# Optimization experiments

Measured on AMD Instinct MI355X. Metric: run time of the kernel, lower is better.

The kernel has to match this reference:

```python
import jax, jax.numpy as jnp
import numpy as np

D_IN, D_OUT, RANK, N = 4096, 4096, 16, 8192


def _quantize_weight(w, bits):
    # round-to-nearest fake quantization, stored back as floats (as in the torch code)
    absmax = jnp.abs(w).max()
    scale = (2 ** (bits - 1) - 1) / absmax
    q = jnp.clip(jnp.round(w * scale), -2 ** (bits - 1), 2 ** (bits - 1) - 1)
    return q / scale


def _double_quantization(w, bits):
    absmax = jnp.abs(w).max()
    c1 = (2 ** (bits - 1) - 1) / absmax          # scalar fp32 scale
    q = jnp.clip(jnp.round(w * c1), -2 ** (bits - 1), 2 ** (bits - 1) - 1)
    return c1, q / c1                             # c_kbit_2 has same shape as w


def setup_inputs() -> dict:
    key = jax.random.key(0)
    kX, kW, kL1, kL2 = jax.random.split(key, 4)
    X = jax.random.normal(kX, (N, D_IN), dtype=jnp.float32)
    W0 = jax.random.normal(kW, (D_IN, D_OUT), dtype=jnp.float32)
    W_nf4 = _quantize_weight(W0, bits=4)
    c_fp32_1, c_kbit_2 = _double_quantization(W_nf4, bits=8)
    L1 = jax.random.normal(kL1, (D_IN, RANK), dtype=jnp.float32)
    L2 = jax.random.normal(kL2, (RANK, D_OUT), dtype=jnp.float32)
    return {"X": X, "W_nf4": W_nf4, "c_fp32_1": c_fp32_1,
            "c_kbit_2": c_kbit_2, "L1": L1, "L2": L2}


def reference(X, W_nf4, c_fp32_1, c_kbit_2, L1, L2):
    # dequantize: elementwise scalar * elementwise-tensor scaling of stored weight
    W = W_nf4 * c_fp32_1 * c_kbit_2               # [D_IN, D_OUT]
    # main GEMM + low-rank LoRA path, added in the epilogue
    Y = X @ W + (X @ L1) @ L2                     # [N, D_OUT]
    return Y
```

## Files before the change

### kernel.cpp

```cpp
#include <hip/hip_runtime.h>


#define M_ROWS 8192
#define K_DIM  4096
#define N_OUT  4096
#define CVT_BLOCKS 16384
#define WP_BLOCKS  4096

typedef float  f32x16 __attribute__((ext_vector_type(16)));
typedef float  f32x4  __attribute__((ext_vector_type(4)));
typedef __bf16 bf16x8 __attribute__((ext_vector_type(8)));
typedef unsigned short ushort8v __attribute__((ext_vector_type(8)));

__device__ float          Tg[(size_t)M_ROWS * 16];
__device__ unsigned short L1t[16 * K_DIM];
__device__ unsigned short L2t[N_OUT * 16];

__device__ __forceinline__ unsigned short f2bf(float f) {
    __bf16 h = (__bf16)f;
    union { __bf16 h; unsigned short u; } v; v.h = h;
    return v.u;
}

__global__ __launch_bounds__(256) void cvt_kernel(
        const float* __restrict__ X, ushort8v* __restrict__ Xh) {
    size_t tid = (size_t)blockIdx.x * 256 + threadIdx.x;
    const float4* xp = (const float4*)X;
    float4 a = xp[tid * 2];
    float4 b = xp[tid * 2 + 1];
    ushort8v o;
    o[0] = f2bf(a.x); o[1] = f2bf(a.y); o[2] = f2bf(a.z); o[3] = f2bf(a.w);
    o[4] = f2bf(b.x); o[5] = f2bf(b.y); o[6] = f2bf(b.z); o[7] = f2bf(b.w);
    Xh[tid] = o;
}

__global__ __launch_bounds__(256) void wprep_kernel(
        const float* __restrict__ Wnf4, const float* __restrict__ c1p,
        const float* __restrict__ c2,   unsigned short* __restrict__ Wt) {
    __shared__ unsigned short tile[64][72];
    const int t  = threadIdx.x;
    const int wb = blockIdx.x;
    const int n0 = (wb & 63) * 64;
    const int k0 = (wb >> 6) * 64;
    const float c1 = *c1p;

    #pragma unroll
    for (int i = 0; i < 4; ++i) {
        int idx = i * 1024 + t * 4;
        int k = idx >> 6, n4 = idx & 63;
        size_t g = (size_t)(k0 + k) * N_OUT + n0 + n4;
        float4 w = *(const float4*)&Wnf4[g];
        float4 s = *(const float4*)&c2[g];
        tile[n4    ][k] = f2bf(w.x * c1 * s.x);
        tile[n4 + 1][k] = f2bf(w.y * c1 * s.y);
        tile[n4 + 2][k] = f2bf(w.z * c1 * s.z);
        tile[n4 + 3][k] = f2bf(w.w * c1 * s.w);
    }
    __syncthreads();

    #pragma unroll
    for (int i = 0; i < 2; ++i) {
        int task = i * 256 + t;
        int n = task >> 3, k8 = (task & 7) * 8;
        ushort8v o = *(const ushort8v*)&tile[n][k8];
        *(ushort8v*)&Wt[(size_t)(n0 + n) * K_DIM + k0 + k8] = o;
    }
}

__global__ __launch_bounds__(256) void lorap_kernel(
        const float* __restrict__ L1, const float* __restrict__ L2) {
    const int idx = blockIdx.x * 256 + threadIdx.x;
    if (idx < K_DIM) {
        const float4* lp = (const float4*)&L1[(size_t)idx * 16];
        float4 r0 = lp[0], r1 = lp[1], r2 = lp[2], r3 = lp[3];
        float v[16] = {r0.x, r0.y, r0.z, r0.w, r1.x, r1.y, r1.z, r1.w,
                       r2.x, r2.y, r2.z, r2.w, r3.x, r3.y, r3.z, r3.w};
        #pragma unroll
        for (int r = 0; r < 16; ++r)
            L1t[(size_t)r * K_DIM + idx] = f2bf(v[r]);
    } else {
        const int n = idx - K_DIM;
        ushort8v a, b;
        #pragma unroll
        for (int r = 0; r < 8; ++r) a[r] = f2bf(L2[(size_t)r * N_OUT + n]);
        #pragma unroll
        for (int r = 0; r < 8; ++r) b[r] = f2bf(L2[(size_t)(r + 8) * N_OUT + n]);
        *(ushort8v*)&L2t[(size_t)n * 16]     = a;
        *(ushort8v*)&L2t[(size_t)n * 16 + 8] = b;
    }
}

__global__ __launch_bounds__(256) void xl1_kernel(const __bf16* __restrict__ Xh) {
    __shared__ float red[4][256];
    const int m0 = blockIdx.x * 16;
    const int t = threadIdx.x, wv = t >> 6, lane = t & 63;
    const int l15 = lane & 15, l4 = lane >> 4;
    const __bf16* ap = Xh + (size_t)(m0 + l15) * K_DIM + wv * 1024 + l4 * 8;
    const __bf16* bp = (const __bf16*)L1t + (size_t)l15 * K_DIM + wv * 1024 + l4 * 8;
    f32x4 acc = {};
    #pragma unroll 8
    for (int k = 0; k < 1024; k += 32) {
        bf16x8 a = *(const bf16x8*)(ap + k);
        bf16x8 b = *(const bf16x8*)(bp + k);
        acc = __builtin_amdgcn_mfma_f32_16x16x32_bf16(a, b, acc, 0, 0, 0);
    }
    #pragma unroll
    for (int r = 0; r < 4; ++r) red[wv][(l4 * 4 + r) * 16 + l15] = acc[r];
    __syncthreads();
    if (wv == 0) {
        #pragma unroll
        for (int r = 0; r < 4; ++r) {
            int e = (l4 * 4 + r) * 16 + l15;
            Tg[(size_t)(m0 + l4 * 4 + r) * 16 + l15] =
                red[0][e] + red[1][e] + red[2][e] + red[3][e];
        }
    }
}

#define COMPUTE(B) do { \
    bf16x8 af[2][2], bf[2][2]; \
    _Pragma("unroll") for (int mt = 0; mt < 2; ++mt) \
      _Pragma("unroll") for (int ks = 0; ks < 2; ++ks) { \
        int row = wm + mt * 32 + l32; \
        int slot = (2 * ks + half) ^ rsw; \
        af[mt][ks] = *(const bf16x8*)(&As[B][0] + row * 32 + slot * 8); \
      } \
    _Pragma("unroll") for (int nt = 0; nt < 2; ++nt) \
      _Pragma("unroll") for (int ks = 0; ks < 2; ++ks) { \
        int row = wn + nt * 32 + l32; \
        int slot = (2 * ks + half) ^ rsw; \
        bf[nt][ks] = *(const bf16x8*)(&Bs[B][0] + row * 32 + slot * 8); \
      } \
    _Pragma("unroll") for (int ks = 0; ks < 2; ++ks) \
      _Pragma("unroll") for (int mt = 0; mt < 2; ++mt) \
        _Pragma("unroll") for (int nt = 0; nt < 2; ++nt) \
          acc[mt][nt] = __builtin_amdgcn_mfma_f32_32x32x16_bf16( \
              af[mt][ks], bf[nt][ks], acc[mt][nt], 0, 0, 0); \
} while (0)

__global__ __launch_bounds__(256) void gemm_bt_kernel(
        const __bf16* __restrict__ A, const __bf16* __restrict__ Bt,
        float* __restrict__ C, int m_base) {
    __shared__ __bf16 As[2][128 * 32];
    __shared__ __bf16 Bs[2][128 * 32];

    const int t    = threadIdx.x;
    const int w    = t >> 6;
    const int lane = t & 63;
    const int half = lane >> 5;
    const int l32  = lane & 31;

    const int m0   = m_base + blockIdx.y * 128;
    const int n0   = blockIdx.x * 128;

    const int wm   = (w >> 1) * 64;
    const int wn   = (w & 1) * 64;

    const int srow = lane >> 2;
    const int scol = ((lane & 3) ^ ((lane >> 3) & 3)) * 8;
    const int rsw = (l32 >> 1) & 3;

    f32x16 acc[2][2] = {};

    for (int kb = 0; kb < K_DIM; kb += 64) {
        __syncthreads();
        #pragma unroll
        for (int b = 0; b < 2; ++b) {
            #pragma unroll
            for (int j = 0; j < 2; ++j) {
                int row = w * 32 + j * 16 + srow;
                const __bf16* gp = A + (size_t)(m0 + row) * K_DIM + kb + b * 32 + scol;
                __builtin_amdgcn_global_load_lds(
                    (const __attribute__((address_space(1))) unsigned int*)gp,
                    (__attribute__((address_space(3))) unsigned int*)
                        (&As[b][0] + (w * 32 + j * 16) * 32),
                    16, 0, 0);
            }
            #pragma unroll
            for (int j = 0; j < 2; ++j) {
                int row = w * 32 + j * 16 + srow;
                const __bf16* gp = Bt + (size_t)(n0 + row) * K_DIM + kb + b * 32 + scol;
                __builtin_amdgcn_global_load_lds(
                    (const __attribute__((address_space(1))) unsigned int*)gp,
                    (__attribute__((address_space(3))) unsigned int*)
                        (&Bs[b][0] + (w * 32 + j * 16) * 32),
                    16, 0, 0);
            }
        }
        __syncthreads();

        COMPUTE(0);
        COMPUTE(1);
    }

    {
        bf16x8 afl[2], bfl[2];
        #pragma unroll
        for (int mt = 0; mt < 2; ++mt) {
            const float* tp = Tg + (size_t)(m0 + wm + mt * 32 + l32) * 16 + half * 8;
            float4 p0 = *(const float4*)tp;
            float4 p1 = *(const float4*)(tp + 4);
            afl[mt][0] = (__bf16)p0.x; afl[mt][1] = (__bf16)p0.y;
            afl[mt][2] = (__bf16)p0.z; afl[mt][3] = (__bf16)p0.w;
            afl[mt][4] = (__bf16)p1.x; afl[mt][5] = (__bf16)p1.y;
            afl[mt][6] = (__bf16)p1.z; afl[mt][7] = (__bf16)p1.w;
        }
        #pragma unroll
        for (int nt = 0; nt < 2; ++nt)
            bfl[nt] = *(const bf16x8*)((const __bf16*)L2t +
                        (size_t)(n0 + wn + nt * 32 + l32) * 16 + half * 8);
        #pragma unroll
        for (int mt = 0; mt < 2; ++mt)
            #pragma unroll
            for (int nt = 0; nt < 2; ++nt)
                acc[mt][nt] = __builtin_amdgcn_mfma_f32_32x32x16_bf16(
                    afl[mt], bfl[nt], acc[mt][nt], 0, 0, 0);
    }

    #pragma unroll
    for (int mt = 0; mt < 2; ++mt)
        #pragma unroll
        for (int nt = 0; nt < 2; ++nt) {
            int col = n0 + wn + nt * 32 + l32;
            #pragma unroll
            for (int reg = 0; reg < 16; ++reg) {
                int row = m0 + wm + mt * 32 + (reg & 3) + 8 * (reg >> 2) + 4 * half;
                C[(size_t)row * N_OUT + col] = acc[mt][nt][reg];
            }
        }
}

extern "C" void kernel_launch(void* const* d_in, const int* in_sizes, int n_in,
                              void* d_out, int out_size, void* d_ws, size_t ws_size,
                              hipStream_t stream) {
    const float* X    = (const float*)d_in[0];
    const float* Wnf4 = (const float*)d_in[1];
    const float* c1   = (const float*)d_in[2];
    const float* c2   = (const float*)d_in[3];
    const float* L1   = (const float*)d_in[4];
    const float* L2   = (const float*)d_in[5];
    float* Y = (float*)d_out;

    unsigned short* Xh = (unsigned short*)d_ws;
    unsigned short* Wt = (unsigned short*)((char*)d_ws + (size_t)M_ROWS * K_DIM * 2);

    cvt_kernel<<<CVT_BLOCKS, 256, 0, stream>>>(X, (ushort8v*)Xh);
    cvt_kernel<<<CVT_BLOCKS, 256, 0, stream>>>(X, (ushort8v*)Xh);
    wprep_kernel<<<WP_BLOCKS, 256, 0, stream>>>(Wnf4, c1, c2, Wt);
    wprep_kernel<<<WP_BLOCKS, 256, 0, stream>>>(Wnf4, c1, c2, Wt);
    lorap_kernel<<<32, 256, 0, stream>>>(L1, L2);
    lorap_kernel<<<32, 256, 0, stream>>>(L1, L2);
    xl1_kernel<<<M_ROWS / 16, 256, 0, stream>>>((const __bf16*)Xh);
    xl1_kernel<<<M_ROWS / 16, 256, 0, stream>>>((const __bf16*)Xh);

    gemm_bt_kernel<<<dim3(N_OUT / 128, 32), 256, 0, stream>>>(
        (const __bf16*)Xh, (const __bf16*)Wt, Y, 0);
    gemm_bt_kernel<<<dim3(N_OUT / 128, 32), 256, 0, stream>>>(
        (const __bf16*)Xh, (const __bf16*)Wt, Y, 4096);
}
```

Baseline: 705.4 us.

## Software-pipeline GEMM K loop, drop duplicate prep launches, split GEMM into eight launches

The GEMM main loop now uses a K step of 32 with double-buffered LDS, issuing the next tile's global-to-LDS loads before computing on the current buffer. This removes the second barrier per iteration and lets loads overlap with MFMA work. Separately, the duplicated launches of the conversion, weight-prep, LoRA-prep and X·L1 kernels are removed, and the GEMM is split into eight launches of 1024 rows instead of two of 4096. There is only one barrier per iteration while the next stage is written into the other buffer; correctness depends on that barrier ordering the loads against the previous compute.

```diff
diff --git a/kernel.cpp b/kernel.cpp
--- a/kernel.cpp
+++ b/kernel.cpp
@@ -118,7 +118,7 @@
 }
 
 #define COMPUTE(B) do { \
-    bf16x8 af[2][2], bf[2][2]; \
+    bf16x8 af[2][2], bfr[2][2]; \
     _Pragma("unroll") for (int mt = 0; mt < 2; ++mt) \
       _Pragma("unroll") for (int ks = 0; ks < 2; ++ks) { \
         int row = wm + mt * 32 + l32; \
@@ -129,13 +129,13 @@
       _Pragma("unroll") for (int ks = 0; ks < 2; ++ks) { \
         int row = wn + nt * 32 + l32; \
         int slot = (2 * ks + half) ^ rsw; \
-        bf[nt][ks] = *(const bf16x8*)(&Bs[B][0] + row * 32 + slot * 8); \
+        bfr[nt][ks] = *(const bf16x8*)(&Bs[B][0] + row * 32 + slot * 8); \
       } \
     _Pragma("unroll") for (int ks = 0; ks < 2; ++ks) \
       _Pragma("unroll") for (int mt = 0; mt < 2; ++mt) \
         _Pragma("unroll") for (int nt = 0; nt < 2; ++nt) \
           acc[mt][nt] = __builtin_amdgcn_mfma_f32_32x32x16_bf16( \
-              af[mt][ks], bf[nt][ks], acc[mt][nt], 0, 0, 0); \
+              af[mt][ks], bfr[nt][ks], acc[mt][nt], 0, 0, 0); \
 } while (0)
 
 __global__ __launch_bounds__(256) void gemm_bt_kernel(
@@ -160,37 +160,33 @@
     const int scol = ((lane & 3) ^ ((lane >> 3) & 3)) * 8;
     const int rsw = (l32 >> 1) & 3;
 
+    auto stg = [&](int b, int kb) {
+        #pragma unroll
+        for (int j = 0; j < 2; ++j) {
+            int row = w * 32 + j * 16 + srow;
+            const __bf16* ga = A + (size_t)(m0 + row) * K_DIM + kb + scol;
+            __builtin_amdgcn_global_load_lds(
+                (const __attribute__((address_space(1))) unsigned int*)ga,
+                (__attribute__((address_space(3))) unsigned int*)
+                    (&As[b][0] + (w * 32 + j * 16) * 32),
+                16, 0, 0);
+            const __bf16* gb = Bt + (size_t)(n0 + row) * K_DIM + kb + scol;
+            __builtin_amdgcn_global_load_lds(
+                (const __attribute__((address_space(1))) unsigned int*)gb,
+                (__attribute__((address_space(3))) unsigned int*)
+                    (&Bs[b][0] + (w * 32 + j * 16) * 32),
+                16, 0, 0);
+        }
+    };
+
     f32x16 acc[2][2] = {};
 
-    for (int kb = 0; kb < K_DIM; kb += 64) {
+    stg(0, 0);
+    for (int kb = 0; kb < K_DIM; kb += 32) {
+        const int cur = (kb >> 5) & 1;
         __syncthreads();
-        #pragma unroll
-        for (int b = 0; b < 2; ++b) {
-            #pragma unroll
-            for (int j = 0; j < 2; ++j) {
-                int row = w * 32 + j * 16 + srow;
-                const __bf16* gp = A + (size_t)(m0 + row) * K_DIM + kb + b * 32 + scol;
-                __builtin_amdgcn_global_load_lds(
-                    (const __attribute__((address_space(1))) unsigned int*)gp,
-                    (__attribute__((address_space(3))) unsigned int*)
-                        (&As[b][0] + (w * 32 + j * 16) * 32),
-                    16, 0, 0);
-            }
-            #pragma unroll
-            for (int j = 0; j < 2; ++j) {
-                int row = w * 32 + j * 16 + srow;
-                const __bf16* gp = Bt + (size_t)(n0 + row) * K_DIM + kb + b * 32 + scol;
-                __builtin_amdgcn_global_load_lds(
-                    (const __attribute__((address_space(1))) unsigned int*)gp,
-                    (__attribute__((address_space(3))) unsigned int*)
-                        (&Bs[b][0] + (w * 32 + j * 16) * 32),
-                    16, 0, 0);
-            }
-        }
-        __syncthreads();
-
-        COMPUTE(0);
-        COMPUTE(1);
+        if (kb + 32 < K_DIM) stg(cur ^ 1, kb + 32);
+        COMPUTE(cur);
     }
 
     {
@@ -245,16 +241,11 @@
     unsigned short* Wt = (unsigned short*)((char*)d_ws + (size_t)M_ROWS * K_DIM * 2);
 
     cvt_kernel<<<CVT_BLOCKS, 256, 0, stream>>>(X, (ushort8v*)Xh);
-    cvt_kernel<<<CVT_BLOCKS, 256, 0, stream>>>(X, (ushort8v*)Xh);
-    wprep_kernel<<<WP_BLOCKS, 256, 0, stream>>>(Wnf4, c1, c2, Wt);
     wprep_kernel<<<WP_BLOCKS, 256, 0, stream>>>(Wnf4, c1, c2, Wt);
     lorap_kernel<<<32, 256, 0, stream>>>(L1, L2);
-    lorap_kernel<<<32, 256, 0, stream>>>(L1, L2);
     xl1_kernel<<<M_ROWS / 16, 256, 0, stream>>>((const __bf16*)Xh);
-    xl1_kernel<<<M_ROWS / 16, 256, 0, stream>>>((const __bf16*)Xh);
-
-    gemm_bt_kernel<<<dim3(N_OUT / 128, 32), 256, 0, stream>>>(
-        (const __bf16*)Xh, (const __bf16*)Wt, Y, 0);
-    gemm_bt_kernel<<<dim3(N_OUT / 128, 32), 256, 0, stream>>>(
-        (const __bf16*)Xh, (const __bf16*)Wt, Y, 4096);
-}
+
+    for (int q = 0; q < 8; ++q)
+        gemm_bt_kernel<<<dim3(N_OUT / 128, 8), 256, 0, stream>>>(
+            (const __bf16*)Xh, (const __bf16*)Wt, Y, q * 1024);
+}
```

Result: slower. 909.8 us (+29.0%).

## Fuse prep kernels into one launch, drop duplicate launches, split GEMM into quarters

Applied to the files above, without the earlier changes.

Merges the X conversion, weight dequant/transpose and X@L1 kernels into a single block-dispatched prep kernel, with the X@L1 part reading fp32 X directly and converting to bf16 in registers. Removes the duplicated launches of every prep kernel. The main GEMM is issued as four launches over 2048-row slices instead of two. This cuts redundant memory traffic and launch overhead, at the cost of heterogeneous blocks sharing one launch and extra fp32 reads of X in the LoRA path.

```diff
diff --git a/kernel.cpp b/kernel.cpp
--- a/kernel.cpp
+++ b/kernel.cpp
@@ -6,6 +6,8 @@
 #define N_OUT  4096
 #define CVT_BLOCKS 16384
 #define WP_BLOCKS  4096
+#define XL1_BLOCKS 512
+#define PREP_BLOCKS (CVT_BLOCKS + WP_BLOCKS + XL1_BLOCKS)
 
 typedef float  f32x16 __attribute__((ext_vector_type(16)));
 typedef float  f32x4  __attribute__((ext_vector_type(4)));
@@ -20,51 +22,6 @@
     __bf16 h = (__bf16)f;
     union { __bf16 h; unsigned short u; } v; v.h = h;
     return v.u;
-}
-
-__global__ __launch_bounds__(256) void cvt_kernel(
-        const float* __restrict__ X, ushort8v* __restrict__ Xh) {
-    size_t tid = (size_t)blockIdx.x * 256 + threadIdx.x;
-    const float4* xp = (const float4*)X;
-    float4 a = xp[tid * 2];
-    float4 b = xp[tid * 2 + 1];
-    ushort8v o;
-    o[0] = f2bf(a.x); o[1] = f2bf(a.y); o[2] = f2bf(a.z); o[3] = f2bf(a.w);
-    o[4] = f2bf(b.x); o[5] = f2bf(b.y); o[6] = f2bf(b.z); o[7] = f2bf(b.w);
-    Xh[tid] = o;
-}
-
-__global__ __launch_bounds__(256) void wprep_kernel(
-        const float* __restrict__ Wnf4, const float* __restrict__ c1p,
-        const float* __restrict__ c2,   unsigned short* __restrict__ Wt) {
-    __shared__ unsigned short tile[64][72];
-    const int t  = threadIdx.x;
-    const int wb = blockIdx.x;
-    const int n0 = (wb & 63) * 64;
-    const int k0 = (wb >> 6) * 64;
-    const float c1 = *c1p;
-
-    #pragma unroll
-    for (int i = 0; i < 4; ++i) {
-        int idx = i * 1024 + t * 4;
-        int k = idx >> 6, n4 = idx & 63;
-        size_t g = (size_t)(k0 + k) * N_OUT + n0 + n4;
-        float4 w = *(const float4*)&Wnf4[g];
-        float4 s = *(const float4*)&c2[g];
-        tile[n4    ][k] = f2bf(w.x * c1 * s.x);
-        tile[n4 + 1][k] = f2bf(w.y * c1 * s.y);
-        tile[n4 + 2][k] = f2bf(w.z * c1 * s.z);
-        tile[n4 + 3][k] = f2bf(w.w * c1 * s.w);
-    }
-    __syncthreads();
-
-    #pragma unroll
-    for (int i = 0; i < 2; ++i) {
-        int task = i * 256 + t;
-        int n = task >> 3, k8 = (task & 7) * 8;
-        ushort8v o = *(const ushort8v*)&tile[n][k8];
-        *(ushort8v*)&Wt[(size_t)(n0 + n) * K_DIM + k0 + k8] = o;
-    }
 }
 
 __global__ __launch_bounds__(256) void lorap_kernel(
@@ -90,35 +47,91 @@
     }
 }
 
-__global__ __launch_bounds__(256) void xl1_kernel(const __bf16* __restrict__ Xh) {
-    __shared__ float red[4][256];
-    const int m0 = blockIdx.x * 16;
-    const int t = threadIdx.x, wv = t >> 6, lane = t & 63;
-    const int l15 = lane & 15, l4 = lane >> 4;
-    const __bf16* ap = Xh + (size_t)(m0 + l15) * K_DIM + wv * 1024 + l4 * 8;
-    const __bf16* bp = (const __bf16*)L1t + (size_t)l15 * K_DIM + wv * 1024 + l4 * 8;
-    f32x4 acc = {};
-    #pragma unroll 8
-    for (int k = 0; k < 1024; k += 32) {
-        bf16x8 a = *(const bf16x8*)(ap + k);
-        bf16x8 b = *(const bf16x8*)(bp + k);
-        acc = __builtin_amdgcn_mfma_f32_16x16x32_bf16(a, b, acc, 0, 0, 0);
-    }
-    #pragma unroll
-    for (int r = 0; r < 4; ++r) red[wv][(l4 * 4 + r) * 16 + l15] = acc[r];
-    __syncthreads();
-    if (wv == 0) {
-        #pragma unroll
-        for (int r = 0; r < 4; ++r) {
-            int e = (l4 * 4 + r) * 16 + l15;
-            Tg[(size_t)(m0 + l4 * 4 + r) * 16 + l15] =
-                red[0][e] + red[1][e] + red[2][e] + red[3][e];
+__global__ __launch_bounds__(256) void prep_all_kernel(
+        const float* __restrict__ X,    ushort8v* __restrict__ Xh,
+        const float* __restrict__ Wnf4, const float* __restrict__ c1p,
+        const float* __restrict__ c2,   unsigned short* __restrict__ Wt) {
+    const int t = threadIdx.x;
+
+    if (blockIdx.x < CVT_BLOCKS) {
+        size_t tid = (size_t)blockIdx.x * 256 + t;
+        const float4* xp = (const float4*)X;
+        float4 a = xp[tid * 2];
+        float4 b = xp[tid * 2 + 1];
+        ushort8v o;
+        o[0] = f2bf(a.x); o[1] = f2bf(a.y); o[2] = f2bf(a.z); o[3] = f2bf(a.w);
+        o[4] = f2bf(b.x); o[5] = f2bf(b.y); o[6] = f2bf(b.z); o[7] = f2bf(b.w);
+        Xh[tid] = o;
+        return;
+    }
+
+    if (blockIdx.x < CVT_BLOCKS + WP_BLOCKS) {
+        __shared__ unsigned short tile[64][72];
+        const int wb = blockIdx.x - CVT_BLOCKS;
+        const int n0 = (wb & 63) * 64;
+        const int k0 = (wb >> 6) * 64;
+        const float c1 = *c1p;
+
+        #pragma unroll
+        for (int i = 0; i < 4; ++i) {
+            int idx = i * 1024 + t * 4;
+            int k = idx >> 6, n4 = idx & 63;
+            size_t g = (size_t)(k0 + k) * N_OUT + n0 + n4;
+            float4 w = *(const float4*)&Wnf4[g];
+            float4 s = *(const float4*)&c2[g];
+            tile[n4    ][k] = f2bf(w.x * c1 * s.x);
+            tile[n4 + 1][k] = f2bf(w.y * c1 * s.y);
+            tile[n4 + 2][k] = f2bf(w.z * c1 * s.z);
+            tile[n4 + 3][k] = f2bf(w.w * c1 * s.w);
+        }
+        __syncthreads();
+
+        #pragma unroll
+        for (int i = 0; i < 2; ++i) {
+            int task = i * 256 + t;
+            int n = task >> 3, k8 = (task & 7) * 8;
+            ushort8v o = *(const ushort8v*)&tile[n][k8];
+            *(ushort8v*)&Wt[(size_t)(n0 + n) * K_DIM + k0 + k8] = o;
+        }
+        return;
+    }
+
+    {
+        __shared__ float red[4][256];
+        const int m0 = (blockIdx.x - CVT_BLOCKS - WP_BLOCKS) * 16;
+        const int wv = t >> 6, lane = t & 63;
+        const int l15 = lane & 15, l4 = lane >> 4;
+        const float* ap = X + (size_t)(m0 + l15) * K_DIM + wv * 1024 + l4 * 8;
+        const __bf16* bp = (const __bf16*)L1t + (size_t)l15 * K_DIM + wv * 1024 + l4 * 8;
+        f32x4 acc = {};
+        #pragma unroll 8
+        for (int k = 0; k < 1024; k += 32) {
+            float4 p0 = *(const float4*)(ap + k);
+            float4 p1 = *(const float4*)(ap + k + 4);
+            bf16x8 a;
+            a[0] = (__bf16)p0.x; a[1] = (__bf16)p0.y;
+            a[2] = (__bf16)p0.z; a[3] = (__bf16)p0.w;
+            a[4] = (__bf16)p1.x; a[5] = (__bf16)p1.y;
+            a[6] = (__bf16)p1.z; a[7] = (__bf16)p1.w;
+            bf16x8 b = *(const bf16x8*)(bp + k);
+            acc = __builtin_amdgcn_mfma_f32_16x16x32_bf16(a, b, acc, 0, 0, 0);
+        }
+        #pragma unroll
+        for (int r = 0; r < 4; ++r) red[wv][(l4 * 4 + r) * 16 + l15] = acc[r];
+        __syncthreads();
+        if (wv == 0) {
+            #pragma unroll
+            for (int r = 0; r < 4; ++r) {
+                int e = (l4 * 4 + r) * 16 + l15;
+                Tg[(size_t)(m0 + l4 * 4 + r) * 16 + l15] =
+                    red[0][e] + red[1][e] + red[2][e] + red[3][e];
+            }
         }
     }
 }
 
 #define COMPUTE(B) do { \
-    bf16x8 af[2][2], bf[2][2]; \
+    bf16x8 af[2][2], bfr[2][2]; \
     _Pragma("unroll") for (int mt = 0; mt < 2; ++mt) \
       _Pragma("unroll") for (int ks = 0; ks < 2; ++ks) { \
         int row = wm + mt * 32 + l32; \
@@ -129,13 +142,13 @@
       _Pragma("unroll") for (int ks = 0; ks < 2; ++ks) { \
         int row = wn + nt * 32 + l32; \
         int slot = (2 * ks + half) ^ rsw; \
-        bf[nt][ks] = *(const bf16x8*)(&Bs[B][0] + row * 32 + slot * 8); \
+        bfr[nt][ks] = *(const bf16x8*)(&Bs[B][0] + row * 32 + slot * 8); \
       } \
     _Pragma("unroll") for (int ks = 0; ks < 2; ++ks) \
       _Pragma("unroll") for (int mt = 0; mt < 2; ++mt) \
         _Pragma("unroll") for (int nt = 0; nt < 2; ++nt) \
           acc[mt][nt] = __builtin_amdgcn_mfma_f32_32x32x16_bf16( \
-              af[mt][ks], bf[nt][ks], acc[mt][nt], 0, 0, 0); \
+              af[mt][ks], bfr[nt][ks], acc[mt][nt], 0, 0, 0); \
 } while (0)
 
 __global__ __launch_bounds__(256) void gemm_bt_kernel(
@@ -244,17 +257,11 @@
     unsigned short* Xh = (unsigned short*)d_ws;
     unsigned short* Wt = (unsigned short*)((char*)d_ws + (size_t)M_ROWS * K_DIM * 2);
 
-    cvt_kernel<<<CVT_BLOCKS, 256, 0, stream>>>(X, (ushort8v*)Xh);
-    cvt_kernel<<<CVT_BLOCKS, 256, 0, stream>>>(X, (ushort8v*)Xh);
-    wprep_kernel<<<WP_BLOCKS, 256, 0, stream>>>(Wnf4, c1, c2, Wt);
-    wprep_kernel<<<WP_BLOCKS, 256, 0, stream>>>(Wnf4, c1, c2, Wt);
     lorap_kernel<<<32, 256, 0, stream>>>(L1, L2);
-    lorap_kernel<<<32, 256, 0, stream>>>(L1, L2);
-    xl1_kernel<<<M_ROWS / 16, 256, 0, stream>>>((const __bf16*)Xh);
-    xl1_kernel<<<M_ROWS / 16, 256, 0, stream>>>((const __bf16*)Xh);
-
-    gemm_bt_kernel<<<dim3(N_OUT / 128, 32), 256, 0, stream>>>(
-        (const __bf16*)Xh, (const __bf16*)Wt, Y, 0);
-    gemm_bt_kernel<<<dim3(N_OUT / 128, 32), 256, 0, stream>>>(
-        (const __bf16*)Xh, (const __bf16*)Wt, Y, 4096);
-}
+    prep_all_kernel<<<PREP_BLOCKS, 256, 0, stream>>>(
+        X, (ushort8v*)Xh, Wnf4, c1, c2, Wt);
+
+    for (int q = 0; q < 4; ++q)
+        gemm_bt_kernel<<<dim3(N_OUT / 128, 16), 256, 0, stream>>>(
+            (const __bf16*)Xh, (const __bf16*)Wt, Y, q * 2048);
+}
```

Result: slower. 720.5 us (+2.1%).
